# Optimization experiments

Measured on AMD Instinct MI355X. Metric: run time of the kernel, lower is better.

## Reference

```python
import jax, jax.numpy as jnp
import numpy as np

N_EMBD = 384
HEAD_SIZE = 16

def setup_inputs() -> dict:
    key = jax.random.key(0)
    k1, k2, k3, k4 = jax.random.split(key, 4)
    B, T = 4, 4096
    x = jax.random.normal(k1, (B, T, N_EMBD), dtype=jnp.float32)
    # nn.Linear(n_embd, head_size, bias=False): y = x @ W^T, W: [head_size, n_embd].
    # Store transposed [n_embd, head_size] for direct matmul.
    s = 1.0 / np.sqrt(N_EMBD)
    Wk = jax.random.uniform(k2, (N_EMBD, HEAD_SIZE), jnp.float32, -s, s)
    Wq = jax.random.uniform(k3, (N_EMBD, HEAD_SIZE), jnp.float32, -s, s)
    Wv = jax.random.uniform(k4, (N_EMBD, HEAD_SIZE), jnp.float32, -s, s)
    return {"x": x, "Wk": Wk, "Wq": Wq, "Wv": Wv}

def reference(x, Wk, Wq, Wv):
    B, T, C = x.shape
    k = x @ Wk  # [B,T,H]
    q = x @ Wq
    v = x @ Wv
    scale = k.shape[-1] ** -0.5
    wei = jnp.einsum('bth,bsh->bts', q, k) * scale  # [B,T,T]
    causal = jnp.tril(jnp.ones((T, T), dtype=bool))
    wei = jnp.where(causal, wei, -jnp.inf)
    wei = jax.nn.softmax(wei, axis=-1)
    out = jnp.einsum('bts,bsh->bth', wei, v)  # [B,T,H]
    return out
```

## Files before the change

### kernel.cpp

```cpp
#include <hip/hip_runtime.h>


constexpr int B_DIM = 4;
constexpr int T_SEQ = 4096;
constexpr int C_DIM = 384;
constexpr int H_DIM = 16;
constexpr int NROW  = B_DIM * T_SEQ;

typedef __bf16 bf16x8 __attribute__((ext_vector_type(8)));
typedef float  f32x4  __attribute__((ext_vector_type(4)));

__device__ __forceinline__ unsigned short f2bf(float f) {
  unsigned int u = __builtin_bit_cast(unsigned int, f);
  u += 0x7fffu + ((u >> 16) & 1u);
  return (unsigned short)(u >> 16);
}
__device__ __forceinline__ bf16x8 as_bf16x8(uint4 u) {
  return __builtin_bit_cast(bf16x8, u);
}

__global__ __launch_bounds__(256) void wconv(
    const float* __restrict__ Wk, const float* __restrict__ Wq,
    const float* __restrict__ Wv, unsigned short* __restrict__ WT) {
  const int i = blockIdx.x * 256 + threadIdx.x;
  const int m = i / 6144;
  const int r = i - m * 6144;
  const int n = r / 384;
  const int k = r - n * 384;
  const float* __restrict__ W = (m == 0) ? Wk : (m == 1) ? Wq : Wv;
  WT[i] = f2bf(W[k * 16 + n]);
}

__global__ __launch_bounds__(128) void qkv_mfma(
    const float* __restrict__ x, const unsigned short* __restrict__ WT,
    unsigned short* __restrict__ Kb,
    unsigned short* __restrict__ Qb,
    unsigned short* __restrict__ VTb)
{
  const int tid  = threadIdx.x;
  const int w    = tid >> 6;
  const int lane = tid & 63;
  const int quad = lane >> 4;
  const int col  = lane & 15;
  const int r0   = blockIdx.x << 4;
  const int kb   = w * 6;

  __shared__ float mrg[12][64];

  const float4* __restrict__ xp =
      reinterpret_cast<const float4*>(x + (size_t)(r0 + col) * C_DIM) + quad * 2;
  float4 araw[12];
#pragma unroll
  for (int kk = 0; kk < 6; ++kk) {
    araw[2 * kk]     = xp[(kb + kk) * 8];
    araw[2 * kk + 1] = xp[(kb + kk) * 8 + 1];
  }

  const uint4* __restrict__ bk = reinterpret_cast<const uint4*>(
      WT + (size_t)col * 384 + quad * 8);
  const uint4* __restrict__ bq = bk + 768;
  const uint4* __restrict__ bv = bk + 1536;

  f32x4 ck = {0.f, 0.f, 0.f, 0.f};
  f32x4 cq = {0.f, 0.f, 0.f, 0.f};
  f32x4 cv = {0.f, 0.f, 0.f, 0.f};
#pragma unroll
  for (int kk = 0; kk < 6; ++kk) {
    uint4 pk;
    const float4 a0 = araw[2 * kk], a1 = araw[2 * kk + 1];
    pk.x = (unsigned)f2bf(a0.x) | ((unsigned)f2bf(a0.y) << 16);
    pk.y = (unsigned)f2bf(a0.z) | ((unsigned)f2bf(a0.w) << 16);
    pk.z = (unsigned)f2bf(a1.x) | ((unsigned)f2bf(a1.y) << 16);
    pk.w = (unsigned)f2bf(a1.z) | ((unsigned)f2bf(a1.w) << 16);
    const bf16x8 av = as_bf16x8(pk);
    ck = __builtin_amdgcn_mfma_f32_16x16x32_bf16(av, as_bf16x8(bk[(kb + kk) * 4]), ck, 0, 0, 0);
    cq = __builtin_amdgcn_mfma_f32_16x16x32_bf16(av, as_bf16x8(bq[(kb + kk) * 4]), cq, 0, 0, 0);
    cv = __builtin_amdgcn_mfma_f32_16x16x32_bf16(av, as_bf16x8(bv[(kb + kk) * 4]), cv, 0, 0, 0);
  }

  if (w == 1) {
#pragma unroll
    for (int r = 0; r < 4; ++r) {
      mrg[r][lane]     = ck[r];
      mrg[4 + r][lane] = cq[r];
      mrg[8 + r][lane] = cv[r];
    }
  }
  __syncthreads();
  if (w == 0) {
    const float SC = 0.25f * 1.44269504088896341f;
#pragma unroll
    for (int r = 0; r < 4; ++r) {
      const float vk = ck[r] + mrg[r][lane];
      const float vq = cq[r] + mrg[4 + r][lane];
      const float vv = cv[r] + mrg[8 + r][lane];
      const int row = r0 + quad * 4 + r;
      Kb[row * 16 + col]      = f2bf(vk);
      Qb[row * 32 + col]      = f2bf(vq * SC);
      Qb[row * 32 + 16 + col] = 0;
      const int bb = row >> 12, t = row & 4095;
      VTb[(((size_t)(bb * 16 + col)) << 12) + t] = f2bf(vv);
    }
  }
}

__global__ __launch_bounds__(256) void flash_v5(
    const unsigned short* __restrict__ Qb,
    const unsigned short* __restrict__ Kb,
    const unsigned short* __restrict__ VTb,
    float* __restrict__ PO, float* __restrict__ PL)
{
  const int tid  = threadIdx.x;
  const int w    = tid >> 6;
  const int lane = tid & 63;
  const int quad = lane >> 4;
  const int col  = lane & 15;
  const int qt   = 255 - (blockIdx.x >> 3);
  const int b    = (blockIdx.x >> 1) & 3;
  const int h    = blockIdx.x & 1;
  const int slot = h * 4 + w;
  const int r0   = qt << 4;

  __shared__ __attribute__((aligned(16))) unsigned short Pl[4][2][16 * 72];

  const uint4* qp = reinterpret_cast<const uint4*>(
      Qb + (((size_t)(b * T_SEQ + r0 + col)) << 5) + quad * 8);
  const bf16x8 qa = as_bf16x8(qp[0]);

  f32x4 o = {0.f, 0.f, 0.f, 0.f};
  float l_[4] = {0.f, 0.f, 0.f, 0.f};

  const unsigned short* Kbase = Kb + ((size_t)(b * T_SEQ) << 4);
  const unsigned short* Vbase = VTb + (((size_t)(b * 16 + col)) << 12);
  const int nch = (qt + 4) >> 2;

  unsigned short* const P0 = Pl[w][0];
  unsigned short* const P1 = Pl[w][1];

  auto computeP = [&](int c, unsigned short* P) {
    const int kt0 = c << 2;
    f32x4 sf[4];
#pragma unroll
    for (int t = 0; t < 4; ++t) {
      const int kt = kt0 + t;
      if (kt <= qt) {
        const uint4* kp = reinterpret_cast<const uint4*>(
            Kbase + (((size_t)(kt * 16 + col)) << 4) + quad * 8);
        f32x4 z = {0.f, 0.f, 0.f, 0.f};
        sf[t] = __builtin_amdgcn_mfma_f32_16x16x32_bf16(qa, as_bf16x8(kp[0]), z, 0, 0, 0);
      } else {
#pragma unroll
        for (int r = 0; r < 4; ++r) sf[t][r] = -1e30f;
      }
    }
    const int td = qt - kt0;
    if (td >= 0 && td < 4) {
#pragma unroll
      for (int r = 0; r < 4; ++r)
        if (col > quad * 4 + r) sf[td][r] = -1e30f;
    }
#pragma unroll
    for (int t = 0; t < 4; ++t) {
#pragma unroll
      for (int r = 0; r < 4; ++r) {
        const float p = __builtin_amdgcn_exp2f(sf[t][r]);
        l_[r] += p;
        P[(quad * 4 + r) * 72 + t * 16 + col] = f2bf(p);
      }
    }
  };

  auto doPV = [&](int c, const unsigned short* P) {
    const uint4 v0 = *reinterpret_cast<const uint4*>(Vbase + c * 64 + quad * 8);
    const uint4 v1 = *reinterpret_cast<const uint4*>(Vbase + c * 64 + 32 + quad * 8);
    const uint4 p0 = *reinterpret_cast<const uint4*>(P + col * 72 + quad * 8);
    const uint4 p1 = *reinterpret_cast<const uint4*>(P + col * 72 + 32 + quad * 8);
    o = __builtin_amdgcn_mfma_f32_16x16x32_bf16(as_bf16x8(p0), as_bf16x8(v0), o, 0, 0, 0);
    o = __builtin_amdgcn_mfma_f32_16x16x32_bf16(as_bf16x8(p1), as_bf16x8(v1), o, 0, 0, 0);
  };

  int c = slot;
  if (c < nch) {
    computeP(c, P0);
    int last = c; c += 8;
    while (c < nch) {
      computeP(c, P1);
      doPV(last, P0);
      last = c; c += 8;
      if (c >= nch) { doPV(last, P1); last = -1; break; }
      computeP(c, P0);
      doPV(last, P1);
      last = c; c += 8;
    }
    if (last >= 0) doPV(last, P0);
  }

#pragma unroll
  for (int d = 1; d < 16; d <<= 1) {
#pragma unroll
    for (int r = 0; r < 4; ++r) l_[r] += __shfl_xor(l_[r], d, 16);
  }

  const size_t rowbase = (size_t)b * T_SEQ + r0;
  float* pO = PO + ((size_t)slot * NROW + rowbase) * 16;
#pragma unroll
  for (int r = 0; r < 4; ++r) {
    pO[(quad * 4 + r) * 16 + col] = o[r];
    if (col == 0) PL[(size_t)slot * NROW + rowbase + quad * 4 + r] = l_[r];
  }
}

__global__ __launch_bounds__(256) void flash_merge(
    const float* __restrict__ PO, const float* __restrict__ PL,
    float* __restrict__ out)
{
  const int i   = blockIdx.x * 256 + threadIdx.x;
  const int row = i >> 4;
  float O = 0.f, L = 0.f;
#pragma unroll
  for (int s = 0; s < 8; ++s) {
    O += PO[((size_t)s * NROW) * 16 + i];
    L += PL[(size_t)s * NROW + row];
  }
  out[i] = O / L;
}

extern "C" void kernel_launch(void* const* d_in, const int* in_sizes, int n_in,
                              void* d_out, int out_size, void* d_ws, size_t ws_size,
                              hipStream_t stream) {
  const float* x  = (const float*)d_in[0];
  const float* Wk = (const float*)d_in[1];
  const float* Wq = (const float*)d_in[2];
  const float* Wv = (const float*)d_in[3];
  float* outp = (float*)d_out;

  unsigned short* Qb  = (unsigned short*)d_ws;
  unsigned short* Kb  = Qb + (size_t)NROW * 32;
  unsigned short* VTb = Kb + (size_t)NROW * 16 + 64;
  unsigned short* WT  = VTb + (size_t)NROW * 16;
  float* PO = (float*)(WT + 18432);
  float* PL = PO + (size_t)8 * NROW * 16;

  wconv<<<72, 256, 0, stream>>>(Wk, Wq, Wv, WT);
  qkv_mfma<<<1024, 128, 0, stream>>>(x, WT, Kb, Qb, VTb);
  flash_v5<<<2048, 256, 0, stream>>>(Qb, Kb, VTb, PO, PL);
  flash_merge<<<1024, 256, 0, stream>>>(PO, PL, outp);
}
```

Measured before the change: 104.0 us.

## Compute transposed scores so P feeds PV MFMA from registers without LDS

The attention kernel now computes S^T = K·Q^T, so each lane's exp'd score fragment already matches the B-operand layout of the P·V MFMA. It packs P to bf16 in registers instead of staging it through shared memory with a double buffer. This removes LDS writes and reads and shrinks the row-sum reduction to two shuffles. It also adds an occupancy hint, uses a packed bf16 conversion intrinsic in the QKV kernel, and vectorises the partial-output store. The cost is a simpler loop without explicit software pipelining, which relies on occupancy to hide load latency.

```diff
diff --git a/kernel.cpp b/kernel.cpp
--- a/kernel.cpp
+++ b/kernel.cpp
@@ -1,4 +1,5 @@
 #include <hip/hip_runtime.h>
+#include <hip/hip_bf16.h>
 
 
 constexpr int B_DIM = 4;
@@ -17,6 +18,13 @@
 }
 __device__ __forceinline__ bf16x8 as_bf16x8(uint4 u) {
   return __builtin_bit_cast(bf16x8, u);
+}
+__device__ __forceinline__ unsigned pk2(float a, float b) {
+  float2 t; t.x = a; t.y = b;
+  __hip_bfloat162 h = __float22bfloat162_rn(t);
+  unsigned u;
+  __builtin_memcpy(&u, &h, 4);
+  return u;
 }
 
 __global__ __launch_bounds__(256) void wconv(
@@ -68,10 +76,10 @@
   for (int kk = 0; kk < 6; ++kk) {
     uint4 pk;
     const float4 a0 = araw[2 * kk], a1 = araw[2 * kk + 1];
-    pk.x = (unsigned)f2bf(a0.x) | ((unsigned)f2bf(a0.y) << 16);
-    pk.y = (unsigned)f2bf(a0.z) | ((unsigned)f2bf(a0.w) << 16);
-    pk.z = (unsigned)f2bf(a1.x) | ((unsigned)f2bf(a1.y) << 16);
-    pk.w = (unsigned)f2bf(a1.z) | ((unsigned)f2bf(a1.w) << 16);
+    pk.x = pk2(a0.x, a0.y);
+    pk.y = pk2(a0.z, a0.w);
+    pk.z = pk2(a1.x, a1.y);
+    pk.w = pk2(a1.z, a1.w);
     const bf16x8 av = as_bf16x8(pk);
     ck = __builtin_amdgcn_mfma_f32_16x16x32_bf16(av, as_bf16x8(bk[(kb + kk) * 4]), ck, 0, 0, 0);
     cq = __builtin_amdgcn_mfma_f32_16x16x32_bf16(av, as_bf16x8(bq[(kb + kk) * 4]), cq, 0, 0, 0);
@@ -104,7 +112,7 @@
   }
 }
 
-__global__ __launch_bounds__(256) void flash_v5(
+__global__ __launch_bounds__(256, 8) void flash_v6(
     const unsigned short* __restrict__ Qb,
     const unsigned short* __restrict__ Kb,
     const unsigned short* __restrict__ VTb,
@@ -117,97 +125,71 @@
   const int col  = lane & 15;
   const int qt   = 255 - (blockIdx.x >> 3);
   const int b    = (blockIdx.x >> 1) & 3;
-  const int h    = blockIdx.x & 1;
-  const int slot = h * 4 + w;
+  const int h2   = blockIdx.x & 1;
+  const int slot = h2 * 4 + w;
   const int r0   = qt << 4;
 
-  __shared__ __attribute__((aligned(16))) unsigned short Pl[4][2][16 * 72];
-
-  const uint4* qp = reinterpret_cast<const uint4*>(
-      Qb + (((size_t)(b * T_SEQ + r0 + col)) << 5) + quad * 8);
-  const bf16x8 qa = as_bf16x8(qp[0]);
+  const bf16x8 qb = as_bf16x8(*reinterpret_cast<const uint4*>(
+      Qb + (((size_t)(b * T_SEQ + r0 + col)) << 5) + quad * 8));
 
   f32x4 o = {0.f, 0.f, 0.f, 0.f};
-  float l_[4] = {0.f, 0.f, 0.f, 0.f};
+  float l = 0.f;
 
   const unsigned short* Kbase = Kb + ((size_t)(b * T_SEQ) << 4);
-  const unsigned short* Vbase = VTb + (((size_t)(b * 16 + col)) << 12);
+  const unsigned short* Vrow  = VTb + (((size_t)(b * 16 + col)) << 12);
   const int nch = (qt + 4) >> 2;
 
-  unsigned short* const P0 = Pl[w][0];
-  unsigned short* const P1 = Pl[w][1];
-
-  auto computeP = [&](int c, unsigned short* P) {
+  for (int c = slot; c < nch; c += 8) {
     const int kt0 = c << 2;
-    f32x4 sf[4];
-#pragma unroll
-    for (int t = 0; t < 4; ++t) {
-      const int kt = kt0 + t;
-      if (kt <= qt) {
-        const uint4* kp = reinterpret_cast<const uint4*>(
+    const bool diag = (kt0 + 4 > qt);
+
+#pragma unroll
+    for (int i = 0; i < 2; ++i) {
+      const int vbase = kt0 * 16 + i * 32 + quad * 4;
+      const uint2 v0 = *reinterpret_cast<const uint2*>(Vrow + vbase);
+      const uint2 v1 = *reinterpret_cast<const uint2*>(Vrow + vbase + 16);
+
+      float p[2][4];
+#pragma unroll
+      for (int t2 = 0; t2 < 2; ++t2) {
+        const int kt = kt0 + 2 * i + t2;
+        const uint4 kf = *reinterpret_cast<const uint4*>(
             Kbase + (((size_t)(kt * 16 + col)) << 4) + quad * 8);
         f32x4 z = {0.f, 0.f, 0.f, 0.f};
-        sf[t] = __builtin_amdgcn_mfma_f32_16x16x32_bf16(qa, as_bf16x8(kp[0]), z, 0, 0, 0);
-      } else {
-#pragma unroll
-        for (int r = 0; r < 4; ++r) sf[t][r] = -1e30f;
+        f32x4 s = __builtin_amdgcn_mfma_f32_16x16x32_bf16(
+            as_bf16x8(kf), qb, z, 0, 0, 0);
+        if (diag) {
+          const int kb0 = kt * 16 + quad * 4 - r0;
+#pragma unroll
+          for (int r = 0; r < 4; ++r)
+            if (kb0 + r > col) s[r] = -1e30f;
+        }
+#pragma unroll
+        for (int r = 0; r < 4; ++r) {
+          p[t2][r] = __builtin_amdgcn_exp2f(s[r]);
+          l += p[t2][r];
+        }
       }
+
+      uint4 pb;
+      pb.x = pk2(p[0][0], p[0][1]);
+      pb.y = pk2(p[0][2], p[0][3]);
+      pb.z = pk2(p[1][0], p[1][1]);
+      pb.w = pk2(p[1][2], p[1][3]);
+      const uint4 va = make_uint4(v0.x, v0.y, v1.x, v1.y);
+      o = __builtin_amdgcn_mfma_f32_16x16x32_bf16(
+          as_bf16x8(va), as_bf16x8(pb), o, 0, 0, 0);
     }
-    const int td = qt - kt0;
-    if (td >= 0 && td < 4) {
-#pragma unroll
-      for (int r = 0; r < 4; ++r)
-        if (col > quad * 4 + r) sf[td][r] = -1e30f;
-    }
-#pragma unroll
-    for (int t = 0; t < 4; ++t) {
-#pragma unroll
-      for (int r = 0; r < 4; ++r) {
-        const float p = __builtin_amdgcn_exp2f(sf[t][r]);
-        l_[r] += p;
-        P[(quad * 4 + r) * 72 + t * 16 + col] = f2bf(p);
-      }
-    }
-  };
-
-  auto doPV = [&](int c, const unsigned short* P) {
-    const uint4 v0 = *reinterpret_cast<const uint4*>(Vbase + c * 64 + quad * 8);
-    const uint4 v1 = *reinterpret_cast<const uint4*>(Vbase + c * 64 + 32 + quad * 8);
-    const uint4 p0 = *reinterpret_cast<const uint4*>(P + col * 72 + quad * 8);
-    const uint4 p1 = *reinterpret_cast<const uint4*>(P + col * 72 + 32 + quad * 8);
-    o = __builtin_amdgcn_mfma_f32_16x16x32_bf16(as_bf16x8(p0), as_bf16x8(v0), o, 0, 0, 0);
-    o = __builtin_amdgcn_mfma_f32_16x16x32_bf16(as_bf16x8(p1), as_bf16x8(v1), o, 0, 0, 0);
-  };
-
-  int c = slot;
-  if (c < nch) {
-    computeP(c, P0);
-    int last = c; c += 8;
-    while (c < nch) {
-      computeP(c, P1);
-      doPV(last, P0);
-      last = c; c += 8;
-      if (c >= nch) { doPV(last, P1); last = -1; break; }
-      computeP(c, P0);
-      doPV(last, P1);
-      last = c; c += 8;
-    }
-    if (last >= 0) doPV(last, P0);
-  }
-
-#pragma unroll
-  for (int d = 1; d < 16; d <<= 1) {
-#pragma unroll
-    for (int r = 0; r < 4; ++r) l_[r] += __shfl_xor(l_[r], d, 16);
-  }
+  }
+
+  l += __shfl_xor(l, 16);
+  l += __shfl_xor(l, 32);
 
   const size_t rowbase = (size_t)b * T_SEQ + r0;
   float* pO = PO + ((size_t)slot * NROW + rowbase) * 16;
-#pragma unroll
-  for (int r = 0; r < 4; ++r) {
-    pO[(quad * 4 + r) * 16 + col] = o[r];
-    if (col == 0) PL[(size_t)slot * NROW + rowbase + quad * 4 + r] = l_[r];
-  }
+  *reinterpret_cast<float4*>(pO + col * 16 + quad * 4) =
+      __builtin_bit_cast(float4, o);
+  if (quad == 0) PL[(size_t)slot * NROW + rowbase + col] = l;
 }
 
 __global__ __launch_bounds__(256) void flash_merge(
@@ -243,6 +225,6 @@
 
   wconv<<<72, 256, 0, stream>>>(Wk, Wq, Wv, WT);
   qkv_mfma<<<1024, 128, 0, stream>>>(x, WT, Kb, Qb, VTb);
-  flash_v5<<<2048, 256, 0, stream>>>(Qb, Kb, VTb, PO, PL);
+  flash_v6<<<2048, 256, 0, stream>>>(Qb, Kb, VTb, PO, PL);
   flash_merge<<<1024, 256, 0, stream>>>(PO, PL, outp);
 }
```

Measured after the change: 106.6 us. 2.5% more time.
